# Kernel tuning notes

Measured on AMD Instinct MI355X. Metric: run time of the kernel, lower is better.

Reference implementation:

```python
import jax, jax.numpy as jnp
import numpy as np

B, L, W, S, STEPS, VOCAB, NLAB = 1024, 128, 512, 8, 12, 32, 10

def setup_inputs() -> dict:
    key = jax.random.key(0)
    ks = jax.random.split(key, 24)
    def nrm(k, shape, scale=0.05):
        return jax.random.normal(k, shape, jnp.float32) * scale
    x = jax.random.randint(ks[0], (B, L), 0, VOCAB)
    embed = nrm(ks[1], (VOCAB, W), 0.1).at[0].set(0.0)  # padding_idx=0
    return {
        'x': x,
        'embed': embed,
        'W_mix': nrm(ks[2], (W, 3 * W)), 'b_mix': jnp.zeros((W,), jnp.float32),
        'W_in': nrm(ks[3], (S, W, 2 * W)), 'b_in': jnp.zeros((S, W), jnp.float32),
        'W_link': nrm(ks[4], (S, W, W)), 'b_link': jnp.zeros((S, W), jnp.float32),
        'W_ih': nrm(ks[5], (S, 3 * W, W)), 'b_ih': jnp.zeros((S, 3 * W), jnp.float32),
        'W_hh': nrm(ks[6], (S, 3 * W, W)), 'b_hh': jnp.zeros((S, 3 * W), jnp.float32),
        'W_gate': nrm(ks[7], (S, 1, W)), 'b_gate': jnp.zeros((S, 1), jnp.float32),
        'phase': nrm(ks[8], (S, W), 0.5), 'prism_gain': jnp.zeros((S, W), jnp.float32),
        'W_delta': nrm(ks[9], (S, W, W)), 'b_delta': jnp.zeros((S, W), jnp.float32),
        'decay_param': jnp.zeros((), jnp.float32),
        'W_out': nrm(ks[10], (NLAB, W)), 'b_out': jnp.zeros((NLAB,), jnp.float32),
    }

def _encode(x, embed, W_mix, b_mix):
    emb = embed[x]                                          # [B,L,W]
    mask = (x != 0).astype(jnp.float32)[..., None]          # [B,L,1]
    summed = (emb * mask).sum(1)
    denom = jnp.maximum(mask.sum(1), 1.0)
    mean = summed / denom
    maxed = jnp.where(mask == 0, -10000.0, emb).max(1)
    maxed = jnp.where(jnp.isfinite(maxed), maxed, 0.0)
    last_idx = jnp.maximum(mask[..., 0].sum(1).astype(jnp.int32) - 1, 0)
    last = jnp.take_along_axis(emb, last_idx[:, None, None], axis=1)[:, 0]
    cat = jnp.concatenate([mean, maxed, last], -1)          # [B,3W]
    return jnp.tanh(cat @ W_mix.T + b_mix)

def _forward(x, embed, W_mix, b_mix, W_in, b_in, W_link, b_link, W_ih, b_ih,
             W_hh, b_hh, W_gate, b_gate, phase, prism_gain, W_delta, b_delta,
             decay_param, W_out, b_out):
    summary = _encode(x, embed, W_mix, b_mix)               # [B,W]
    decay = jax.nn.sigmoid(decay_param)
    inv_sqrt_s = np.float32(1.0 / np.sqrt(S))
    gain = jax.nn.softplus(prism_gain)[None]                # [1,S,W]

    def step(carry, _):
        h, hs = carry
        shared = jnp.concatenate([h, summary], -1)          # conditioned: [B,2W]
        f0 = jnp.tanh(jnp.einsum('swi,bi->bsw', W_in, shared) + b_in)      # [B,S,W]
        prev = jnp.roll(f0, 1, axis=1)                      # sparse ring: feats[(i-1)%S]
        feats = jnp.tanh(f0 + jnp.einsum('sow,bsw->bso', W_link, prev) + b_link)
        # recurrent side pockets: per-side GRUCell (torch gate order r,z,n)
        gi = jnp.einsum('sgw,bsw->bsg', W_ih, feats) + b_ih
        gh = jnp.einsum('sgw,bsw->bsg', W_hh, hs) + b_hh
        ir, iz, inn = jnp.split(gi, 3, -1)
        hr, hz, hn = jnp.split(gh, 3, -1)
        r = jax.nn.sigmoid(ir + hr)
        z = jax.nn.sigmoid(iz + hz)
        n = jnp.tanh(inn + r * hn)
        hs_new = (1.0 - z) * n + z * hs                     # [B,S,W]
        feat = hs_new
        gate = jax.nn.sigmoid(jnp.einsum('sow,bsw->bso', W_gate, feat) + b_gate)  # [B,S,1]
        feat = jnp.cos(feat + phase[None]) ** 2 * gain      # prismion
        upd = gate * jnp.tanh(jnp.einsum('sow,bsw->bso', W_delta, feat) + b_delta)
        delta = upd.sum(1) * inv_sqrt_s
        h_new = jnp.tanh(h * decay + delta)
        return (h_new, hs_new), None

    hs0 = jnp.zeros((B, S, W), jnp.float32)
    (h, _), _ = jax.lax.scan(step, (summary, hs0), None, length=STEPS)
    return h @ W_out.T + b_out                               # [B,10]

def reference(x, embed, W_mix, b_mix, W_in, b_in, W_link, b_link, W_ih, b_ih,
              W_hh, b_hh, W_gate, b_gate, phase, prism_gain, W_delta, b_delta,
              decay_param, W_out, b_out):
    return _forward(x, embed, W_mix, b_mix, W_in, b_in, W_link, b_link, W_ih,
                    b_ih, W_hh, b_hh, W_gate, b_gate, phase, prism_gain,
                    W_delta, b_delta, decay_param, W_out, b_out)
```

## Files before the change

kernel.cpp:

```cpp
#include <hip/hip_runtime.h>
#include <hip/hip_bf16.h>


typedef unsigned short u16;
typedef __attribute__((ext_vector_type(8))) short short8;
typedef __attribute__((ext_vector_type(4))) float f32x4;

__device__ __forceinline__ float bf2f(u16 v) {
    union { unsigned int u; float f; } x; x.u = ((unsigned int)v) << 16; return x.f;
}
__device__ __forceinline__ u16 f2bf(float f) {
    union { float f; unsigned int u; } x; x.f = f;
    unsigned int u = x.u;
    return (u16)((u + 0x7FFFu + ((u >> 16) & 1u)) >> 16);
}
__device__ __forceinline__ float fsig(float v) {
    return __builtin_amdgcn_rcpf(1.f + __expf(-v));
}
__device__ __forceinline__ float ftanh(float v) {
    return 1.f - 2.f * __builtin_amdgcn_rcpf(__expf(2.f * v) + 1.f);
}
__device__ __forceinline__ float fsoftplus(float v) {
    return (v > 20.f) ? v : __logf(1.f + __expf(v));
}

union U4 { ushort4 v; u16 e[4]; };

__device__ __forceinline__ void gload_lds16(const u16* g, u16* l) {
    __builtin_amdgcn_global_load_lds(
        (const __attribute__((address_space(1))) unsigned int*)g,
        (__attribute__((address_space(3))) unsigned int*)l, 16, 0, 0);
}

__device__ __forceinline__ int sane16(u16 u) {
    if ((u & 0x7FFF) == 0) return 1;
    int e = (u >> 7) & 0xFF;
    return (e >= 0x33 && e <= 0x43) ? 1 : 0;
}
__global__ __launch_bounds__(256) void detect_k(const u16* __restrict__ raw,
                                                int* __restrict__ flag) {
    const int t = threadIdx.x;
    int c = sane16(raw[1024 + t * 2]) + sane16(raw[1024 + t * 2 + 1]);
#pragma unroll
    for (int off = 32; off; off >>= 1) c += __shfl_down(c, off, 64);
    __shared__ int red[4];
    if ((t & 63) == 0) red[t >> 6] = c;
    __syncthreads();
    if (t == 0) *flag = (red[0] + red[1] + red[2] + red[3] >= 448) ? 1 : 0;
}

struct CT { const void* src[20]; int n[20]; int off[20]; };
__global__ __launch_bounds__(256) void conv_k(CT ct, u16* __restrict__ dstBase,
                                              const int* __restrict__ flag) {
    const int isbf = *flag;
    const int gid = blockIdx.x * 256 + threadIdx.x;
    const int stride = gridDim.x * 256;
    for (int tn = 0; tn < 20; ++tn) {
        const int n = ct.n[tn];
        const int n4 = n >> 2;
        u16* dst = dstBase + ct.off[tn];
        if (!isbf) {
            const float* s = (const float*)ct.src[tn];
            for (int i = gid; i < n4; i += stride) {
                f32x4 v = *(const f32x4*)(s + i * 4);
                *(ushort4*)(dst + i * 4) =
                    make_ushort4(f2bf(v[0]), f2bf(v[1]), f2bf(v[2]), f2bf(v[3]));
            }
            if (gid < (n & 3)) { int i = n4 * 4 + gid; dst[i] = f2bf(s[i]); }
        } else {
            const u16* s = (const u16*)ct.src[tn];
            for (int i = gid; i < n4; i += stride)
                *(ushort4*)(dst + i * 4) = *(const ushort4*)(s + i * 4);
            if (gid < (n & 3)) { int i = n4 * 4 + gid; dst[i] = s[i]; }
        }
    }
}

__global__ __launch_bounds__(256) void pack_k(const u16* __restrict__ Wih,
                                              const u16* __restrict__ Whh,
                                              u16* __restrict__ Wcat) {
    long i = ((long)blockIdx.x * 256 + threadIdx.x) * 8;
    if (i >= 8L * 1536 * 512) return;
    long sg = i >> 9;
    long k  = i & 511;
    *(short8*)(Wcat + sg * 1024 + k)       = *(const short8*)(Wih + i);
    *(short8*)(Wcat + sg * 1024 + 512 + k) = *(const short8*)(Whh + i);
}

struct GP {
    const u16* A;  long lda; long aOff[8];
    const u16* Bw; long ldb; long bwOff[8];
    const u16* bias; long biasOff[8];
    const u16* add; long ldadd; long addOff;
    const float* gate_pre;
    const u16* bgate;
    void* C; long ldc; long cOff[8];
    float* C2;
    u16* C3;
    int K; int nt;
};

template<int EPI, int MT, int SWZ>
__global__ __launch_bounds__(256) void gemm_k(GP p) {
    constexpr int MW   = MT / 32;
    constexpr int AITS = MT / 32;
    __shared__ __align__(16) u16 lA[2][MT * 64];
    __shared__ __align__(16) u16 lB[2][128 * 64];
    const int t    = threadIdx.x;
    const int lane = t & 63;
    const int wv   = t >> 6;
    int bx = blockIdx.x, byy = blockIdx.y;
    if (SWZ) {
        int wgid = bx + (byy << 5);
        bx  = ((wgid & 7) << 2) + ((wgid >> 3) & 3);
        byy = wgid >> 5;
    }
    const int z    = bx / p.nt;
    const int n0   = (bx - z * p.nt) * 128;
    const int m0   = byy * MT;

    const u16* Ab = p.A + p.aOff[z] + (long)m0 * p.lda;
    const u16* Bb = p.Bw + p.bwOff[z] + (long)n0 * p.ldb;

    f32x4 acc[MW][4];
#pragma unroll
    for (int i = 0; i < MW; i++)
#pragma unroll
        for (int j = 0; j < 4; j++) acc[i][j] = (f32x4){0.f, 0.f, 0.f, 0.f};

    const int wm   = (wv & 1) * (MT / 2);
    const int wn   = (wv >> 1) * 64;
    const int fr   = lane & 15;
    const int quad = lane >> 4;

    const int nk = p.K >> 6;
#pragma unroll
    for (int it = 0; it < AITS; ++it) {
        int flat = it * 256 + t, row = flat >> 3, src = (flat & 7) ^ (row & 7);
        gload_lds16(Ab + (long)row * p.lda + src * 8, &lA[0][flat * 8]);
    }
#pragma unroll
    for (int it = 0; it < 4; ++it) {
        int flat = it * 256 + t, row = flat >> 3, src = (flat & 7) ^ (row & 7);
        gload_lds16(Bb + (long)row * p.ldb + src * 8, &lB[0][flat * 8]);
    }
    __syncthreads();

    for (int kt = 0; kt < nk; ++kt) {
        const int cur = kt & 1, nxt = cur ^ 1;
        if (kt + 1 < nk) {
            const long kb = (long)(kt + 1) * 64;
#pragma unroll
            for (int it = 0; it < AITS; ++it) {
                int flat = it * 256 + t, row = flat >> 3, src = (flat & 7) ^ (row & 7);
                gload_lds16(Ab + (long)row * p.lda + kb + src * 8, &lA[nxt][flat * 8]);
            }
#pragma unroll
            for (int it = 0; it < 4; ++it) {
                int flat = it * 256 + t, row = flat >> 3, src = (flat & 7) ^ (row & 7);
                gload_lds16(Bb + (long)row * p.ldb + kb + src * 8, &lB[nxt][flat * 8]);
            }
        }
#pragma unroll
        for (int kk = 0; kk < 2; ++kk) {
            const int q = kk * 4 + quad;
            short8 aF[MW], bF[4];
#pragma unroll
            for (int mi = 0; mi < MW; mi++) {
                int row = wm + mi * 16 + fr;
                aF[mi] = *(const short8*)&lA[cur][row * 64 + (q ^ (row & 7)) * 8];
            }
#pragma unroll
            for (int ni = 0; ni < 4; ni++) {
                int row = wn + ni * 16 + fr;
                bF[ni] = *(const short8*)&lB[cur][row * 64 + (q ^ (row & 7)) * 8];
            }
#pragma unroll
            for (int mi = 0; mi < MW; mi++)
#pragma unroll
                for (int ni = 0; ni < 4; ni++)
                    acc[mi][ni] = __builtin_amdgcn_mfma_f32_16x16x32_bf16(
                        aF[mi], bF[ni], acc[mi][ni], 0, 0, 0);
        }
        __syncthreads();
    }

    float sgv[MW][4];
    if (EPI == 3) {
#pragma unroll
        for (int mi = 0; mi < MW; mi++)
#pragma unroll
            for (int r = 0; r < 4; r++) {
                long row = m0 + wm + mi * 16 + quad * 4 + r;
                sgv[mi][r] = fsig(p.gate_pre[row * 8 + z] + bf2f(p.bgate[z]));
            }
    }

#pragma unroll
    for (int mi = 0; mi < MW; mi++) {
#pragma unroll
        for (int ni = 0; ni < 4; ni++) {
            const int mg = m0 + wm + mi * 16 + quad * 4;
            const int ng = n0 + wn + ni * 16 + fr;
#pragma unroll
            for (int r = 0; r < 4; r++) {
                float v = acc[mi][ni][r];
                const long row = mg + r;
                if (EPI == 1) {
                    float ad = bf2f(p.add[z * p.addOff + row * p.ldadd + ng]);
                    v = ftanh(v + ad + bf2f(p.bias[p.biasOff[z] + ng]));
                    ((u16*)p.C)[p.cOff[z] + row * p.ldc + ng] = f2bf(v);
                } else if (EPI == 3) {
                    v = ftanh(v + bf2f(p.bias[p.biasOff[z] + ng])) * sgv[mi][r];
                    ((u16*)p.C)[p.cOff[z] + row * p.ldc + ng] = f2bf(v);
                } else if (EPI == 4) {
                    v = ftanh(v + bf2f(p.bias[ng]));
                    u16 b = f2bf(v);
                    ((u16*)p.C)[row * 512 + ng] = b;
                    p.C3[row * 512 + ng] = b;
                    p.C2[row * 512 + ng] = v;
                } else if (EPI == 6) {
                    v = v + bf2f(p.bias[p.biasOff[z] + ng]);
                    ((u16*)p.C)[p.cOff[z] + row * p.ldc + ng] = f2bf(v);
                } else {
                    float ad = bf2f(p.add[row * p.ldadd + ng]);
                    v = ftanh(v + ad);
                    ((u16*)p.C)[row * p.ldc + ng] = f2bf(v);
                }
            }
        }
    }
}

struct GGP {
    const u16* fhs_in;
    u16* fhs_out;
    const u16* Wcat;
    const u16* b_ih;
    const u16* b_hh;
    u16* prism;
    float* gate_pre;
    const u16* Wg;
    const u16* phase;
    const u16* pgain;
};

__global__ __launch_bounds__(256, 2) void grug_k(GGP p) {
    __shared__ __align__(16) u16 sA[2][64 * 32];
    __shared__ __align__(16) u16 sW[2][3][128 * 32];
    const int t    = threadIdx.x;
    const int lane = t & 63;
    const int wv   = t >> 6;
    const int wgid = blockIdx.x + (blockIdx.y << 5);
    const int s    = wgid & 7;
    const int idx  = wgid >> 3;
    const int w0   = (idx & 3) * 128;
    const int m0   = (idx >> 2) * 64;
    const int fr   = lane & 15;
    const int quad = lane >> 4;
    const int wn   = wv * 32;

    const u16* Ab = p.fhs_in + (long)m0 * 8192 + s * 1024;
    const u16* Wb = p.Wcat + (long)s * 1536 * 1024;

    f32x4 acc[4][4][2];
#pragma unroll
    for (int q = 0; q < 4; q++)
#pragma unroll
        for (int mi = 0; mi < 4; mi++)
#pragma unroll
            for (int ni = 0; ni < 2; ni++) acc[q][mi][ni] = (f32x4){0.f,0.f,0.f,0.f};

    const int arow = t >> 2, ac4 = t & 3, asrc = ac4 ^ ((arow >> 1) & 3);

    auto stageA = [&](int buf, long kb) {
        gload_lds16(Ab + (long)arow * 8192 + kb + asrc * 8, &sA[buf][t * 8]);
    };
    auto stageW = [&](int buf, long kb) {
#pragma unroll
        for (int q = 0; q < 3; q++)
#pragma unroll
            for (int it = 0; it < 2; ++it) {
                int flat = it * 256 + t, row = flat >> 2, src = (flat & 3) ^ ((row >> 1) & 3);
                long g = (long)(q * 512 + w0 + row);
                gload_lds16(Wb + g * 1024 + kb + src * 8, &sW[buf][q][flat * 8]);
            }
    };

    stageA(0, 0); stageW(0, 0);
    __syncthreads();

    for (int kt = 0; kt < 32; ++kt) {
        const int cur = kt & 1, nxt = cur ^ 1;
        if (kt + 1 < 32) { stageA(nxt, (long)(kt + 1) * 32); stageW(nxt, (long)(kt + 1) * 32); }
        const int qsel = (kt < 16) ? 2 : 3;
        short8 aF[4], bF[3][2];
#pragma unroll
        for (int mi = 0; mi < 4; mi++) {
            int row = mi * 16 + fr;
            aF[mi] = *(const short8*)&sA[cur][row * 32 + ((quad ^ ((row >> 1) & 3)) & 3) * 8];
        }
#pragma unroll
        for (int q = 0; q < 3; q++)
#pragma unroll
            for (int ni = 0; ni < 2; ni++) {
                int row = wn + ni * 16 + fr;
                bF[q][ni] = *(const short8*)&sW[cur][q][row * 32 + ((quad ^ ((row >> 1) & 3)) & 3) * 8];
            }
#pragma unroll
        for (int mi = 0; mi < 4; mi++)
#pragma unroll
            for (int ni = 0; ni < 2; ni++) {
                acc[0][mi][ni] = __builtin_amdgcn_mfma_f32_16x16x32_bf16(aF[mi], bF[0][ni], acc[0][mi][ni], 0, 0, 0);
                acc[1][mi][ni] = __builtin_amdgcn_mfma_f32_16x16x32_bf16(aF[mi], bF[1][ni], acc[1][mi][ni], 0, 0, 0);
                if (qsel == 2)
                    acc[2][mi][ni] = __builtin_amdgcn_mfma_f32_16x16x32_bf16(aF[mi], bF[2][ni], acc[2][mi][ni], 0, 0, 0);
                else
                    acc[3][mi][ni] = __builtin_amdgcn_mfma_f32_16x16x32_bf16(aF[mi], bF[2][ni], acc[3][mi][ni], 0, 0, 0);
            }
        __syncthreads();
    }

    const u16* bih = p.b_ih + (long)s * 1536;
    const u16* bhh = p.b_hh + (long)s * 1536;
    float gp[4][4];
#pragma unroll
    for (int mi = 0; mi < 4; mi++)
#pragma unroll
        for (int r = 0; r < 4; r++) gp[mi][r] = 0.f;

#pragma unroll
    for (int ni = 0; ni < 2; ni++) {
        const int col = w0 + wn + ni * 16 + fr;
        const float br  = bf2f(bih[col])        + bf2f(bhh[col]);
        const float bz  = bf2f(bih[512 + col])  + bf2f(bhh[512 + col]);
        const float bin = bf2f(bih[1024 + col]);
        const float bhn = bf2f(bhh[1024 + col]);
        const float ph  = bf2f(p.phase[s * 512 + col]);
        const float gain = fsoftplus(bf2f(p.pgain[s * 512 + col]));
        const float wg  = bf2f(p.Wg[s * 512 + col]);
#pragma unroll
        for (int mi = 0; mi < 4; mi++) {
#pragma unroll
            for (int r = 0; r < 4; r++) {
                const long b = m0 + mi * 16 + quad * 4 + r;
                float rv = fsig(acc[0][mi][ni][r] + br);
                float zv = fsig(acc[1][mi][ni][r] + bz);
                float nv = ftanh(acc[2][mi][ni][r] + bin + rv * (acc[3][mi][ni][r] + bhn));
                float hold = bf2f(p.fhs_in[b * 8192 + s * 1024 + 512 + col]);
                float hv = (1.f - zv) * nv + zv * hold;
                p.fhs_out[b * 8192 + s * 1024 + 512 + col] = f2bf(hv);
                float c = __cosf(hv + ph);
                p.prism[b * 4096 + s * 512 + col] = f2bf(c * c * gain);
                gp[mi][r] += wg * hv;
            }
        }
    }
#pragma unroll
    for (int m = 1; m < 16; m <<= 1)
#pragma unroll
        for (int mi = 0; mi < 4; mi++)
#pragma unroll
            for (int r = 0; r < 4; r++) gp[mi][r] += __shfl_xor(gp[mi][r], m, 64);
    if (fr == 0) {
#pragma unroll
        for (int mi = 0; mi < 4; mi++)
#pragma unroll
            for (int r = 0; r < 4; r++) {
                long b = m0 + mi * 16 + quad * 4 + r;
                atomicAdd(&p.gate_pre[b * 8 + s], gp[mi][r]);
            }
    }
}

__global__ __launch_bounds__(256) void encode_k(const int* __restrict__ x,
                                                const u16* __restrict__ embed,
                                                u16* __restrict__ cat) {
    __shared__ int toks[128];
    __shared__ int cnt_s;
    const int b = blockIdx.x, t = threadIdx.x;
    if (t < 128) toks[t] = x[b * 128 + t];
    __syncthreads();
    if (t == 0) {
        int c = 0;
        for (int l = 0; l < 128; l++) c += (toks[l] != 0);
        cnt_s = c;
    }
    __syncthreads();
    const int cnt = cnt_s;
    const int lastTok = toks[cnt > 0 ? cnt - 1 : 0];
    for (int w = t; w < 512; w += 256) {
        float sum = 0.f, mx = -10000.f;
        for (int l = 0; l < 128; l++) {
            int tok = toks[l];
            if (tok != 0) {
                float e = bf2f(embed[tok * 512 + w]);
                sum += e;
                mx = fmaxf(mx, e);
            }
        }
        float mean = sum / (float)(cnt > 0 ? cnt : 1);
        float last = bf2f(embed[lastTok * 512 + w]);
        cat[(long)b * 1536 + w]        = f2bf(mean);
        cat[(long)b * 1536 + 512 + w]  = f2bf(mx);
        cat[(long)b * 1536 + 1024 + w] = f2bf(last);
    }
}

__global__ __launch_bounds__(256) void hupd_k(const u16* __restrict__ upd,
                                              float* __restrict__ h,
                                              u16* __restrict__ h_b,
                                              const u16* __restrict__ decay_p) {
    const int idx = blockIdx.x * 256 + threadIdx.x;
    const int b = idx >> 9, w = idx & 511;
    const long base = (long)b * 4096 + w;
    float dsum = 0.f;
#pragma unroll
    for (int s = 0; s < 8; s++) dsum += bf2f(upd[base + s * 512]);
    const float decay = fsig(bf2f(decay_p[0]));
    const float hv = ftanh(h[idx] * decay + dsum * 0.35355339059327373f);
    h[idx] = hv;
    h_b[idx] = f2bf(hv);
}

__global__ __launch_bounds__(64) void out_k(const float* __restrict__ h,
                                            const u16* __restrict__ Wout,
                                            const u16* __restrict__ bout,
                                            void* __restrict__ out,
                                            const int* __restrict__ flag) {
    const int b = blockIdx.x, lane = threadIdx.x;
    const int isbf = *flag;
    for (int j = 0; j < 10; j++) {
        float p = 0.f;
#pragma unroll
        for (int k = 0; k < 8; k++) {
            int w = lane + k * 64;
            p += h[(long)b * 512 + w] * bf2f(Wout[j * 512 + w]);
        }
#pragma unroll
        for (int off = 32; off; off >>= 1) p += __shfl_down(p, off, 64);
        if (lane == 0) {
            float val = p + bf2f(bout[j]);
            if (isbf) ((u16*)out)[b * 10 + j] = f2bf(val);
            else      ((float*)out)[b * 10 + j] = val;
        }
    }
}

extern "C" void kernel_launch(void* const* d_in, const int* in_sizes, int n_in,
                              void* d_out, int out_size, void* d_ws, size_t ws_size,
                              hipStream_t stream) {
    (void)n_in; (void)out_size; (void)ws_size;
    const int* x = (const int*)d_in[0];

    char* pp = (char*)d_ws;
    auto carve = [&](size_t n) { char* r = pp; pp += (n + 255) & ~(size_t)255; return (void*)r; };

    CT ct;
    size_t ctot = 0;
    for (int i = 0; i < 20; i++) {
        ct.src[i] = d_in[i + 1];
        ct.n[i]   = in_sizes[i + 1];
        ct.off[i] = (int)ctot;
        ctot += ((size_t)in_sizes[i + 1] + 15) & ~(size_t)15;
    }
    u16* canon = (u16*)carve(ctot * 2);
    const u16* embed  = canon + ct.off[0];
    const u16* W_mix  = canon + ct.off[1];
    const u16* b_mix  = canon + ct.off[2];
    const u16* W_in   = canon + ct.off[3];
    const u16* b_in   = canon + ct.off[4];
    const u16* W_link = canon + ct.off[5];
    const u16* b_link = canon + ct.off[6];
    const u16* W_ih   = canon + ct.off[7];
    const u16* b_ih   = canon + ct.off[8];
    const u16* W_hh   = canon + ct.off[9];
    const u16* b_hh   = canon + ct.off[10];
    const u16* W_gate = canon + ct.off[11];
    const u16* b_gate = canon + ct.off[12];
    const u16* phase  = canon + ct.off[13];
    const u16* pgain  = canon + ct.off[14];
    const u16* W_delta= canon + ct.off[15];
    const u16* b_delta= canon + ct.off[16];
    const u16* decayp = canon + ct.off[17];
    const u16* W_out  = canon + ct.off[18];
    const u16* b_out  = canon + ct.off[19];

    int*   flag   = (int*)  carve(256);
    u16*   Wcat   = (u16*)  carve((size_t)8 * 1536 * 1024 * 2);
    u16*   cat    = (u16*)  carve((size_t)1024 * 1536 * 2);
    u16*   h_b    = (u16*)  carve((size_t)1024 * 512 * 2);
    u16*   summ_b = (u16*)  carve((size_t)1024 * 512 * 2);
    float* h      = (float*)carve((size_t)1024 * 512 * 4);
    u16*   cin    = (u16*)  carve((size_t)1024 * 4096 * 2);
    u16*   f0     = (u16*)  carve((size_t)1024 * 4096 * 2);
    u16*   fhs0   = (u16*)  carve((size_t)1024 * 8192 * 2);
    u16*   fhs1   = (u16*)  carve((size_t)1024 * 8192 * 2);
    u16*   prism  = (u16*)  carve((size_t)1024 * 4096 * 2);
    u16*   upd    = (u16*)  carve((size_t)1024 * 4096 * 2);
    float* gate_pre = (float*)carve((size_t)1024 * 8 * 4);

    (void)hipMemsetAsync(fhs0, 0, (size_t)1024 * 8192 * 2, stream);
    (void)hipMemsetAsync(fhs1, 0, (size_t)1024 * 8192 * 2, stream);

    detect_k<<<dim3(1), dim3(256), 0, stream>>>((const u16*)d_in[1], flag);
    conv_k<<<dim3(1024), dim3(256), 0, stream>>>(ct, canon, flag);
    pack_k<<<dim3(3072), dim3(256), 0, stream>>>(W_ih, W_hh, Wcat);
    encode_k<<<dim3(1024), dim3(256), 0, stream>>>(x, embed, cat);

    {
        GP p{}; p.A = cat; p.lda = 1536; p.Bw = W_mix; p.ldb = 1536;
        p.bias = b_mix; p.C = h_b; p.ldc = 512; p.C2 = h; p.C3 = summ_b;
        p.K = 1536; p.nt = 4;
        gemm_k<4, 64, 0><<<dim3(4, 16, 1), dim3(256), 0, stream>>>(p);
    }
    {
        GP p{}; p.A = summ_b; p.lda = 512; p.Bw = W_in + 512; p.ldb = 1024;
        p.bias = b_in; p.C = cin; p.ldc = 4096; p.K = 512; p.nt = 32;
        gemm_k<6, 64, 1><<<dim3(32, 16, 1), dim3(256), 0, stream>>>(p);
    }

    for (int step = 0; step < 12; ++step) {
        u16* fhs_cur = (step & 1) ? fhs1 : fhs0;
        u16* fhs_nxt = (step & 1) ? fhs0 : fhs1;
        {
            GP p{}; p.A = h_b; p.lda = 512; p.Bw = W_in; p.ldb = 1024;
            p.add = cin; p.ldadd = 4096; p.C = f0; p.ldc = 4096;
            p.K = 512; p.nt = 32;
            gemm_k<7, 64, 1><<<dim3(32, 16, 1), dim3(256), 0, stream>>>(p);
        }
        {
            GP p{}; p.A = f0; p.lda = 4096;
            for (int s = 0; s < 8; s++) p.aOff[s] = (long)((s + 7) & 7) * 512;
            p.Bw = W_link; p.ldb = 512;
            for (int s = 0; s < 8; s++) p.bwOff[s] = (long)s * 512 * 512;
            p.bias = b_link;
            for (int s = 0; s < 8; s++) p.biasOff[s] = (long)s * 512;
            p.add = f0; p.ldadd = 4096; p.addOff = 512;
            p.C = fhs_cur; p.ldc = 8192;
            for (int s = 0; s < 8; s++) p.cOff[s] = (long)s * 1024;
            p.K = 512; p.nt = 4;
            gemm_k<1, 64, 1><<<dim3(32, 16, 1), dim3(256), 0, stream>>>(p);
        }
        (void)hipMemsetAsync(gate_pre, 0, (size_t)1024 * 8 * 4, stream);
        {
            GGP g{};
            g.fhs_in = fhs_cur; g.fhs_out = fhs_nxt; g.Wcat = Wcat;
            g.b_ih = b_ih; g.b_hh = b_hh; g.prism = prism; g.gate_pre = gate_pre;
            g.Wg = W_gate; g.phase = phase; g.pgain = pgain;
            grug_k<<<dim3(32, 16, 1), dim3(256), 0, stream>>>(g);
        }
        {
            GP p{}; p.A = prism; p.lda = 4096;
            for (int s = 0; s < 8; s++) p.aOff[s] = (long)s * 512;
            p.Bw = W_delta; p.ldb = 512;
            for (int s = 0; s < 8; s++) p.bwOff[s] = (long)s * 512 * 512;
            p.bias = b_delta;
            for (int s = 0; s < 8; s++) p.biasOff[s] = (long)s * 512;
            p.gate_pre = gate_pre; p.bgate = b_gate;
            p.C = upd; p.ldc = 4096;
            for (int s = 0; s < 8; s++) p.cOff[s] = (long)s * 512;
            p.K = 512; p.nt = 4;
            gemm_k<3, 64, 1><<<dim3(32, 16, 1), dim3(256), 0, stream>>>(p);
        }
        hupd_k<<<dim3(2048), dim3(256), 0, stream>>>(upd, h, h_b, decayp);
    }

    out_k<<<dim3(1024), dim3(64), 0, stream>>>(h, W_out, b_out, d_out, flag);
}
```

Before: 1.539 ms.

## Triple-buffer weight tiles with prefetch distance two and partial vmcnt waits

The GRU GEMM kernel's weight tiles move from a double-buffered to a triple-buffered LDS ring, so the W tile for step kt+2 is fetched while step kt computes. The A tile stays double-buffered. The full __syncthreads is replaced by explicit s_waitcnt vmcnt(6) plus s_barrier, so the newest in-flight loads stay pending across the barrier. This hides more global-load latency but uses more LDS, which may reduce occupancy, and it depends on hand-counted vmcnt values being correct.

```diff
diff --git a/kernel.cpp b/kernel.cpp
--- a/kernel.cpp
+++ b/kernel.cpp
@@ -247,7 +247,7 @@
 
 __global__ __launch_bounds__(256, 2) void grug_k(GGP p) {
     __shared__ __align__(16) u16 sA[2][64 * 32];
-    __shared__ __align__(16) u16 sW[2][3][128 * 32];
+    __shared__ __align__(16) u16 sW[3][3][128 * 32];
     const int t    = threadIdx.x;
     const int lane = t & 63;
     const int wv   = t >> 6;
@@ -273,39 +273,44 @@
 
     const int arow = t >> 2, ac4 = t & 3, asrc = ac4 ^ ((arow >> 1) & 3);
 
-    auto stageA = [&](int buf, long kb) {
-        gload_lds16(Ab + (long)arow * 8192 + kb + asrc * 8, &sA[buf][t * 8]);
+    auto stageA = [&](int buf, int kt) {
+        gload_lds16(Ab + (long)arow * 8192 + kt * 32 + asrc * 8, &sA[buf][t * 8]);
     };
-    auto stageW = [&](int buf, long kb) {
+    auto stageW = [&](int buf, int kt) {
 #pragma unroll
         for (int q = 0; q < 3; q++)
 #pragma unroll
             for (int it = 0; it < 2; ++it) {
                 int flat = it * 256 + t, row = flat >> 2, src = (flat & 3) ^ ((row >> 1) & 3);
                 long g = (long)(q * 512 + w0 + row);
-                gload_lds16(Wb + g * 1024 + kb + src * 8, &sW[buf][q][flat * 8]);
+                gload_lds16(Wb + g * 1024 + kt * 32 + src * 8, &sW[buf][q][flat * 8]);
             }
     };
 
-    stageA(0, 0); stageW(0, 0);
-    __syncthreads();
-
+    stageA(0, 0); stageW(0, 0); stageW(1, 1);
+    asm volatile("s_waitcnt vmcnt(6)" ::: "memory");
+    __builtin_amdgcn_s_barrier();
+
+    int aCur = 0, wCur = 0;
     for (int kt = 0; kt < 32; ++kt) {
-        const int cur = kt & 1, nxt = cur ^ 1;
-        if (kt + 1 < 32) { stageA(nxt, (long)(kt + 1) * 32); stageW(nxt, (long)(kt + 1) * 32); }
+        if (kt + 1 < 32) stageA(aCur ^ 1, kt + 1);
+        if (kt + 2 < 32) {
+            int wN = wCur + 2; if (wN >= 3) wN -= 3;
+            stageW(wN, kt + 2);
+        }
         const int qsel = (kt < 16) ? 2 : 3;
         short8 aF[4], bF[3][2];
 #pragma unroll
         for (int mi = 0; mi < 4; mi++) {
             int row = mi * 16 + fr;
-            aF[mi] = *(const short8*)&sA[cur][row * 32 + ((quad ^ ((row >> 1) & 3)) & 3) * 8];
+            aF[mi] = *(const short8*)&sA[aCur][row * 32 + ((quad ^ ((row >> 1) & 3)) & 3) * 8];
         }
 #pragma unroll
         for (int q = 0; q < 3; q++)
 #pragma unroll
             for (int ni = 0; ni < 2; ni++) {
                 int row = wn + ni * 16 + fr;
-                bF[q][ni] = *(const short8*)&sW[cur][q][row * 32 + ((quad ^ ((row >> 1) & 3)) & 3) * 8];
+                bF[q][ni] = *(const short8*)&sW[wCur][q][row * 32 + ((quad ^ ((row >> 1) & 3)) & 3) * 8];
             }
 #pragma unroll
         for (int mi = 0; mi < 4; mi++)
@@ -318,7 +323,13 @@
                 else
                     acc[3][mi][ni] = __builtin_amdgcn_mfma_f32_16x16x32_bf16(aF[mi], bF[2][ni], acc[3][mi][ni], 0, 0, 0);
             }
-        __syncthreads();
+        if (kt < 31) {
+            if (kt == 30) asm volatile("s_waitcnt vmcnt(0) lgkmcnt(0)" ::: "memory");
+            else          asm volatile("s_waitcnt vmcnt(6) lgkmcnt(0)" ::: "memory");
+            __builtin_amdgcn_s_barrier();
+        }
+        aCur ^= 1;
+        wCur += 1; if (wCur >= 3) wCur -= 3;
     }
 
     const u16* bih = p.b_ih + (long)s * 1536;
```

Measured after the change: 1.603 ms. +4.1%, slower.

## Load GRU GEMM fragments directly from global memory, fold gate_pre reset into hupd

Applied to the files above, without the earlier changes.

The fused GRU GEMM kernel no longer stages A and W tiles through shared memory with async copies and barriers. Each wave now loads its MFMA fragments straight from global memory into double-buffered registers, and the k-loop is fully unrolled. This removes LDS traffic and per-iteration __syncthreads, but the A tile is now fetched redundantly by all four waves, the access pattern is less coalesced, and register pressure rises under the 2-waves-per-SIMD launch bound. Separately, the per-step memset of gate_pre is replaced by zeroing it inside hupd_k, plus one memset before the loop, which saves one operation per step.

```diff
diff --git a/kernel.cpp b/kernel.cpp
--- a/kernel.cpp
+++ b/kernel.cpp
@@ -246,8 +246,6 @@
 };
 
 __global__ __launch_bounds__(256, 2) void grug_k(GGP p) {
-    __shared__ __align__(16) u16 sA[2][64 * 32];
-    __shared__ __align__(16) u16 sW[2][3][128 * 32];
     const int t    = threadIdx.x;
     const int lane = t & 63;
     const int wv   = t >> 6;
@@ -260,9 +258,20 @@
     const int quad = lane >> 4;
     const int wn   = wv * 32;
 
-    const u16* Ab = p.fhs_in + (long)m0 * 8192 + s * 1024;
+    const u16* Ab = p.fhs_in + (long)m0 * 8192 + (long)s * 1024;
     const u16* Wb = p.Wcat + (long)s * 1536 * 1024;
 
+    const u16* pA[4];
+#pragma unroll
+    for (int mi = 0; mi < 4; mi++)
+        pA[mi] = Ab + (long)(mi * 16 + fr) * 8192 + quad * 8;
+    const u16* pB[3][2];
+#pragma unroll
+    for (int q = 0; q < 3; q++)
+#pragma unroll
+        for (int ni = 0; ni < 2; ni++)
+            pB[q][ni] = Wb + (long)(q * 512 + w0 + wn + ni * 16 + fr) * 1024 + quad * 8;
+
     f32x4 acc[4][4][2];
 #pragma unroll
     for (int q = 0; q < 4; q++)
@@ -271,54 +280,40 @@
 #pragma unroll
             for (int ni = 0; ni < 2; ni++) acc[q][mi][ni] = (f32x4){0.f,0.f,0.f,0.f};
 
-    const int arow = t >> 2, ac4 = t & 3, asrc = ac4 ^ ((arow >> 1) & 3);
-
-    auto stageA = [&](int buf, long kb) {
-        gload_lds16(Ab + (long)arow * 8192 + kb + asrc * 8, &sA[buf][t * 8]);
-    };
-    auto stageW = [&](int buf, long kb) {
-#pragma unroll
-        for (int q = 0; q < 3; q++)
-#pragma unroll
-            for (int it = 0; it < 2; ++it) {
-                int flat = it * 256 + t, row = flat >> 2, src = (flat & 3) ^ ((row >> 1) & 3);
-                long g = (long)(q * 512 + w0 + row);
-                gload_lds16(Wb + g * 1024 + kb + src * 8, &sW[buf][q][flat * 8]);
-            }
-    };
-
-    stageA(0, 0); stageW(0, 0);
-    __syncthreads();
-
+    short8 aF[2][4];
+    short8 bF[2][3][2];
+#pragma unroll
+    for (int mi = 0; mi < 4; mi++) aF[0][mi] = *(const short8*)(pA[mi]);
+#pragma unroll
+    for (int q = 0; q < 3; q++)
+#pragma unroll
+        for (int ni = 0; ni < 2; ni++) bF[0][q][ni] = *(const short8*)(pB[q][ni]);
+
+#pragma unroll
     for (int kt = 0; kt < 32; ++kt) {
         const int cur = kt & 1, nxt = cur ^ 1;
-        if (kt + 1 < 32) { stageA(nxt, (long)(kt + 1) * 32); stageW(nxt, (long)(kt + 1) * 32); }
-        const int qsel = (kt < 16) ? 2 : 3;
-        short8 aF[4], bF[3][2];
-#pragma unroll
-        for (int mi = 0; mi < 4; mi++) {
-            int row = mi * 16 + fr;
-            aF[mi] = *(const short8*)&sA[cur][row * 32 + ((quad ^ ((row >> 1) & 3)) & 3) * 8];
-        }
-#pragma unroll
-        for (int q = 0; q < 3; q++)
+        if (kt + 1 < 32) {
+            const int off = (kt + 1) * 32;
+#pragma unroll
+            for (int mi = 0; mi < 4; mi++)
+                aF[nxt][mi] = *(const short8*)(pA[mi] + off);
+#pragma unroll
+            for (int q = 0; q < 3; q++)
+#pragma unroll
+                for (int ni = 0; ni < 2; ni++)
+                    bF[nxt][q][ni] = *(const short8*)(pB[q][ni] + off);
+        }
+#pragma unroll
+        for (int mi = 0; mi < 4; mi++)
 #pragma unroll
             for (int ni = 0; ni < 2; ni++) {
-                int row = wn + ni * 16 + fr;
-                bF[q][ni] = *(const short8*)&sW[cur][q][row * 32 + ((quad ^ ((row >> 1) & 3)) & 3) * 8];
-            }
-#pragma unroll
-        for (int mi = 0; mi < 4; mi++)
-#pragma unroll
-            for (int ni = 0; ni < 2; ni++) {
-                acc[0][mi][ni] = __builtin_amdgcn_mfma_f32_16x16x32_bf16(aF[mi], bF[0][ni], acc[0][mi][ni], 0, 0, 0);
-                acc[1][mi][ni] = __builtin_amdgcn_mfma_f32_16x16x32_bf16(aF[mi], bF[1][ni], acc[1][mi][ni], 0, 0, 0);
-                if (qsel == 2)
-                    acc[2][mi][ni] = __builtin_amdgcn_mfma_f32_16x16x32_bf16(aF[mi], bF[2][ni], acc[2][mi][ni], 0, 0, 0);
+                acc[0][mi][ni] = __builtin_amdgcn_mfma_f32_16x16x32_bf16(aF[cur][mi], bF[cur][0][ni], acc[0][mi][ni], 0, 0, 0);
+                acc[1][mi][ni] = __builtin_amdgcn_mfma_f32_16x16x32_bf16(aF[cur][mi], bF[cur][1][ni], acc[1][mi][ni], 0, 0, 0);
+                if (kt < 16)
+                    acc[2][mi][ni] = __builtin_amdgcn_mfma_f32_16x16x32_bf16(aF[cur][mi], bF[cur][2][ni], acc[2][mi][ni], 0, 0, 0);
                 else
-                    acc[3][mi][ni] = __builtin_amdgcn_mfma_f32_16x16x32_bf16(aF[mi], bF[2][ni], acc[3][mi][ni], 0, 0, 0);
-            }
-        __syncthreads();
+                    acc[3][mi][ni] = __builtin_amdgcn_mfma_f32_16x16x32_bf16(aF[cur][mi], bF[cur][2][ni], acc[3][mi][ni], 0, 0, 0);
+            }
     }
 
     const u16* bih = p.b_ih + (long)s * 1536;
@@ -410,8 +405,10 @@
 __global__ __launch_bounds__(256) void hupd_k(const u16* __restrict__ upd,
                                               float* __restrict__ h,
                                               u16* __restrict__ h_b,
-                                              const u16* __restrict__ decay_p) {
+                                              const u16* __restrict__ decay_p,
+                                              float* __restrict__ gate_pre) {
     const int idx = blockIdx.x * 256 + threadIdx.x;
+    if (idx < 8192) gate_pre[idx] = 0.f;
     const int b = idx >> 9, w = idx & 511;
     const long base = (long)b * 4096 + w;
     float dsum = 0.f;
@@ -502,6 +499,7 @@
 
     (void)hipMemsetAsync(fhs0, 0, (size_t)1024 * 8192 * 2, stream);
     (void)hipMemsetAsync(fhs1, 0, (size_t)1024 * 8192 * 2, stream);
+    (void)hipMemsetAsync(gate_pre, 0, (size_t)1024 * 8 * 4, stream);
 
     detect_k<<<dim3(1), dim3(256), 0, stream>>>((const u16*)d_in[1], flag);
     conv_k<<<dim3(1024), dim3(256), 0, stream>>>(ct, canon, flag);
@@ -542,7 +540,6 @@
             p.K = 512; p.nt = 4;
             gemm_k<1, 64, 1><<<dim3(32, 16, 1), dim3(256), 0, stream>>>(p);
         }
-        (void)hipMemsetAsync(gate_pre, 0, (size_t)1024 * 8 * 4, stream);
         {
             GGP g{};
             g.fhs_in = fhs_cur; g.fhs_out = fhs_nxt; g.Wcat = Wcat;
@@ -563,7 +560,7 @@
             p.K = 512; p.nt = 4;
             gemm_k<3, 64, 1><<<dim3(32, 16, 1), dim3(256), 0, stream>>>(p);
         }
-        hupd_k<<<dim3(2048), dim3(256), 0, stream>>>(upd, h, h_b, decayp);
+        hupd_k<<<dim3(2048), dim3(256), 0, stream>>>(upd, h, h_b, decayp, gate_pre);
     }
 
     out_k<<<dim3(1024), dim3(64), 0, stream>>>(h, W_out, b_out, d_out, flag);
```

Result: slower. 2.010 ms (+30.6%).

## Triple-buffer GEMM K-loop with compile-time trip count and fold gate_pre memset into hupd

Applied to the files above, without the earlier changes.

Adds a pipelined gemm_k variant that triple-buffers the LDS tiles, prefetches two k-tiles ahead, and uses explicit vmcnt waits and raw barriers in place of __syncthreads. The K-loop trip count becomes a compile-time constant and is fully unrolled. Separately, the per-step hipMemsetAsync of gate_pre is replaced by zeroing inside hupd_k, plus one initial memset, which removes a memset launch from each of the 12 steps. The extra buffer raises LDS use per block, which may lower occupancy, and the hand-set vmcnt counts must match the number of loads issued per stage.

```diff
diff --git a/kernel.cpp b/kernel.cpp
--- a/kernel.cpp
+++ b/kernel.cpp
@@ -100,12 +100,13 @@
     int K; int nt;
 };
 
-template<int EPI, int MT, int SWZ>
+template<int EPI, int MT, int SWZ, int PIPE, int NK>
 __global__ __launch_bounds__(256) void gemm_k(GP p) {
     constexpr int MW   = MT / 32;
     constexpr int AITS = MT / 32;
-    __shared__ __align__(16) u16 lA[2][MT * 64];
-    __shared__ __align__(16) u16 lB[2][128 * 64];
+    constexpr int NBUF = PIPE ? 3 : 2;
+    __shared__ __align__(16) u16 lA[NBUF][MT * 64];
+    __shared__ __align__(16) u16 lB[NBUF][128 * 64];
     const int t    = threadIdx.x;
     const int lane = t & 63;
     const int wv   = t >> 6;
@@ -133,34 +134,19 @@
     const int fr   = lane & 15;
     const int quad = lane >> 4;
 
-    const int nk = p.K >> 6;
-#pragma unroll
-    for (int it = 0; it < AITS; ++it) {
-        int flat = it * 256 + t, row = flat >> 3, src = (flat & 7) ^ (row & 7);
-        gload_lds16(Ab + (long)row * p.lda + src * 8, &lA[0][flat * 8]);
-    }
-#pragma unroll
-    for (int it = 0; it < 4; ++it) {
-        int flat = it * 256 + t, row = flat >> 3, src = (flat & 7) ^ (row & 7);
-        gload_lds16(Bb + (long)row * p.ldb + src * 8, &lB[0][flat * 8]);
-    }
-    __syncthreads();
-
-    for (int kt = 0; kt < nk; ++kt) {
-        const int cur = kt & 1, nxt = cur ^ 1;
-        if (kt + 1 < nk) {
-            const long kb = (long)(kt + 1) * 64;
-#pragma unroll
-            for (int it = 0; it < AITS; ++it) {
-                int flat = it * 256 + t, row = flat >> 3, src = (flat & 7) ^ (row & 7);
-                gload_lds16(Ab + (long)row * p.lda + kb + src * 8, &lA[nxt][flat * 8]);
-            }
-#pragma unroll
-            for (int it = 0; it < 4; ++it) {
-                int flat = it * 256 + t, row = flat >> 3, src = (flat & 7) ^ (row & 7);
-                gload_lds16(Bb + (long)row * p.ldb + kb + src * 8, &lB[nxt][flat * 8]);
-            }
-        }
+    auto stage = [&](int buf, long kb) {
+#pragma unroll
+        for (int it = 0; it < AITS; ++it) {
+            int flat = it * 256 + t, row = flat >> 3, src = (flat & 7) ^ (row & 7);
+            gload_lds16(Ab + (long)row * p.lda + kb + src * 8, &lA[buf][flat * 8]);
+        }
+#pragma unroll
+        for (int it = 0; it < 4; ++it) {
+            int flat = it * 256 + t, row = flat >> 3, src = (flat & 7) ^ (row & 7);
+            gload_lds16(Bb + (long)row * p.ldb + kb + src * 8, &lB[buf][flat * 8]);
+        }
+    };
+    auto inner = [&](int cur) {
 #pragma unroll
         for (int kk = 0; kk < 2; ++kk) {
             const int q = kk * 4 + quad;
@@ -182,7 +168,34 @@
                     acc[mi][ni] = __builtin_amdgcn_mfma_f32_16x16x32_bf16(
                         aF[mi], bF[ni], acc[mi][ni], 0, 0, 0);
         }
+    };
+
+    if (PIPE == 0) {
+        const int nk = p.K >> 6;
+        stage(0, 0);
         __syncthreads();
+        for (int kt = 0; kt < nk; ++kt) {
+            const int cur = kt & 1, nxt = cur ^ 1;
+            if (kt + 1 < nk) stage(nxt, (long)(kt + 1) * 64);
+            inner(cur);
+            __syncthreads();
+        }
+    } else {
+        stage(0, 0); stage(1, 64);
+        asm volatile("s_waitcnt vmcnt(6)" ::: "memory");
+        __builtin_amdgcn_s_barrier();
+#pragma unroll
+        for (int kt = 0; kt < NK; ++kt) {
+            if (kt + 2 < NK) stage((kt + 2) % 3, (long)(kt + 2) * 64);
+            inner(kt % 3);
+            if (kt + 1 < NK) {
+                if (kt + 2 < NK)
+                    asm volatile("s_waitcnt vmcnt(6) lgkmcnt(0)" ::: "memory");
+                else
+                    asm volatile("s_waitcnt vmcnt(0) lgkmcnt(0)" ::: "memory");
+                __builtin_amdgcn_s_barrier();
+            }
+        }
     }
 
     float sgv[MW][4];
@@ -410,8 +423,10 @@
 __global__ __launch_bounds__(256) void hupd_k(const u16* __restrict__ upd,
                                               float* __restrict__ h,
                                               u16* __restrict__ h_b,
-                                              const u16* __restrict__ decay_p) {
+                                              const u16* __restrict__ decay_p,
+                                              float* __restrict__ gate_pre) {
     const int idx = blockIdx.x * 256 + threadIdx.x;
+    if (idx < 8192) gate_pre[idx] = 0.f;
     const int b = idx >> 9, w = idx & 511;
     const long base = (long)b * 4096 + w;
     float dsum = 0.f;
@@ -502,6 +517,7 @@
 
     (void)hipMemsetAsync(fhs0, 0, (size_t)1024 * 8192 * 2, stream);
     (void)hipMemsetAsync(fhs1, 0, (size_t)1024 * 8192 * 2, stream);
+    (void)hipMemsetAsync(gate_pre, 0, (size_t)1024 * 8 * 4, stream);
 
     detect_k<<<dim3(1), dim3(256), 0, stream>>>((const u16*)d_in[1], flag);
     conv_k<<<dim3(1024), dim3(256), 0, stream>>>(ct, canon, flag);
@@ -512,12 +528,12 @@
         GP p{}; p.A = cat; p.lda = 1536; p.Bw = W_mix; p.ldb = 1536;
         p.bias = b_mix; p.C = h_b; p.ldc = 512; p.C2 = h; p.C3 = summ_b;
         p.K = 1536; p.nt = 4;
-        gemm_k<4, 64, 0><<<dim3(4, 16, 1), dim3(256), 0, stream>>>(p);
+        gemm_k<4, 64, 0, 0, 0><<<dim3(4, 16, 1), dim3(256), 0, stream>>>(p);
     }
     {
         GP p{}; p.A = summ_b; p.lda = 512; p.Bw = W_in + 512; p.ldb = 1024;
         p.bias = b_in; p.C = cin; p.ldc = 4096; p.K = 512; p.nt = 32;
-        gemm_k<6, 64, 1><<<dim3(32, 16, 1), dim3(256), 0, stream>>>(p);
+        gemm_k<6, 64, 1, 1, 8><<<dim3(32, 16, 1), dim3(256), 0, stream>>>(p);
     }
 
     for (int step = 0; step < 12; ++step) {
@@ -527,7 +543,7 @@
             GP p{}; p.A = h_b; p.lda = 512; p.Bw = W_in; p.ldb = 1024;
             p.add = cin; p.ldadd = 4096; p.C = f0; p.ldc = 4096;
             p.K = 512; p.nt = 32;
-            gemm_k<7, 64, 1><<<dim3(32, 16, 1), dim3(256), 0, stream>>>(p);
+            gemm_k<7, 64, 1, 1, 8><<<dim3(32, 16, 1), dim3(256), 0, stream>>>(p);
         }
         {
             GP p{}; p.A = f0; p.lda = 4096;
@@ -540,9 +556,8 @@
             p.C = fhs_cur; p.ldc = 8192;
             for (int s = 0; s < 8; s++) p.cOff[s] = (long)s * 1024;
             p.K = 512; p.nt = 4;
-            gemm_k<1, 64, 1><<<dim3(32, 16, 1), dim3(256), 0, stream>>>(p);
-        }
-        (void)hipMemsetAsync(gate_pre, 0, (size_t)1024 * 8 * 4, stream);
+            gemm_k<1, 64, 1, 1, 8><<<dim3(32, 16, 1), dim3(256), 0, stream>>>(p);
+        }
         {
             GGP g{};
             g.fhs_in = fhs_cur; g.fhs_out = fhs_nxt; g.Wcat = Wcat;
@@ -561,9 +576,9 @@
             p.C = upd; p.ldc = 4096;
             for (int s = 0; s < 8; s++) p.cOff[s] = (long)s * 512;
             p.K = 512; p.nt = 4;
-            gemm_k<3, 64, 1><<<dim3(32, 16, 1), dim3(256), 0, stream>>>(p);
-        }
-        hupd_k<<<dim3(2048), dim3(256), 0, stream>>>(upd, h, h_b, decayp);
+            gemm_k<3, 64, 1, 1, 8><<<dim3(32, 16, 1), dim3(256), 0, stream>>>(p);
+        }
+        hupd_k<<<dim3(2048), dim3(256), 0, stream>>>(upd, h, h_b, decayp, gate_pre);
     }
 
     out_k<<<dim3(1024), dim3(64), 0, stream>>>(h, W_out, b_out, d_out, flag);
```

Result: no change. 1.534 ms (-0.3%).
